# Optimization experiments

Hardware: AMD Instinct MI355X
Metric: run time of the kernel (lower is better)

Reference implementation:

```python
import jax, jax.numpy as jnp
import numpy as np

B, N, D = 4, 2048, 1024
H, DH = 16, 64
MAX_POS_EMB = 256
TOPK = 64


def setup_inputs() -> dict:
    key = jax.random.key(0)
    ks = jax.random.split(key, 8)
    s = 0.02
    inner = H * DH
    return {
        "x": jax.random.normal(ks[0], (B, N, D), jnp.float32),
        "gating_mask": jax.random.uniform(ks[1], (B, 1, N, 1), jnp.float32),
        "Wq": jax.random.normal(ks[2], (D, inner), jnp.float32) * s,
        "bq": jnp.zeros((inner,), jnp.float32),
        "Wkv": jax.random.normal(ks[3], (D, 2 * inner), jnp.float32) * s,
        "bkv": jnp.zeros((2 * inner,), jnp.float32),
        "Wo": jax.random.normal(ks[4], (inner, D), jnp.float32) * s,
        "bo": jnp.zeros((D,), jnp.float32),
        "rel_emb": jax.random.normal(ks[5], (MAX_POS_EMB, DH), jnp.float32) * s,
        "mask": jnp.ones((B, N), bool),
        "sparse_topk": TOPK,
    }


def reference(x, gating_mask, Wq, bq, Wkv, bkv, Wo, bo, rel_emb, mask, sparse_topk):
    b, n, d = x.shape
    h, dh = H, DH
    scale = dh ** -0.5
    mask_val = -jnp.finfo(x.dtype).max

    # projections -> [b, h, n, dh]
    q = (x @ Wq + bq).reshape(b, n, h, dh).transpose(0, 2, 1, 3)
    kv = x @ Wkv + bkv
    k = kv[..., : h * dh].reshape(b, n, h, dh).transpose(0, 2, 1, 3)
    v = kv[..., h * dh:].reshape(b, n, h, dh).transpose(0, 2, 1, 3)

    dots = jnp.einsum("bhid,bhjd->bhij", q, k) * scale  # [b,h,n,n]

    # relative positional bias: q . E[clip(i-j+M, 0, M-1)]
    seq = jnp.arange(n)
    dist = jnp.clip(seq[:, None] - seq[None, :] + MAX_POS_EMB, 0, MAX_POS_EMB - 1)
    qE = jnp.einsum("bhid,rd->bhir", q, rel_emb) * scale  # [b,h,n,R]
    pos_attn = jnp.take_along_axis(qE, dist[None, None, :, :], axis=-1)  # [b,h,n,n]
    dots = dots + pos_attn

    # padding mask: mask_i * mask_j
    full_mask = mask[:, None, :, None] & mask[:, None, None, :]
    dots = jnp.where(full_mask, dots, mask_val)

    # topk sparsification: keep only scores >= k-th largest per row
    top = jax.lax.top_k(dots, sparse_topk)[0]  # [b,h,n,topk]
    vk = top[..., -1:]
    dots = jnp.where(dots < vk, mask_val, dots)

    attn = jax.nn.softmax(dots, axis=-1)
    attn = attn * gating_mask

    out = jnp.einsum("bhij,bhjd->bhid", attn, v)
    out = out.transpose(0, 2, 1, 3).reshape(b, n, h * dh)
    return out @ Wo + bo
```

## Files before the change

kernel.cpp:

```cpp
#include <hip/hip_runtime.h>
#include <stdint.h>


typedef __attribute__((ext_vector_type(8))) short short8;
typedef __attribute__((ext_vector_type(4))) float floatx4;

#define Bn   4
#define Nn   2048
#define Hn   16
#define BHn  (Bn*Hn)
#define DELTA 0.00125f

__device__ __forceinline__ float bf2f(unsigned short u) {
  union { unsigned int i; float f; } v; v.i = ((unsigned int)u) << 16; return v.f;
}
__device__ __forceinline__ unsigned short f2bf(float f) {
  union { float f; unsigned int i; } v; v.f = f;
  unsigned int r = v.i + 0x7fffu + ((v.i >> 16) & 1u);
  return (unsigned short)(r >> 16);
}
__device__ __forceinline__ floatx4 mfma16(short8 a, short8 b, floatx4 c) {
  return __builtin_amdgcn_mfma_f32_16x16x32_bf16(a, b, c, 0, 0, 0);
}
__device__ __forceinline__ void split2(float x, unsigned short& h, unsigned short& m) {
  h = f2bf(x);
  m = f2bf(x - bf2f(h));
}
__device__ __forceinline__ void split3(float x, unsigned short& h, unsigned short& m, unsigned short& l) {
  h = f2bf(x);
  float r = x - bf2f(h);
  m = f2bf(r);
  l = f2bf(r - bf2f(m));
}

__global__ __launch_bounds__(256)
void transpose_split3(const float* __restrict__ W,
                      unsigned short* __restrict__ T0,
                      unsigned short* __restrict__ T1,
                      unsigned short* __restrict__ T2,
                      int K, int Ncols)
{
  __shared__ float tile[32][33];
  int k0 = blockIdx.y * 32, n0 = blockIdx.x * 32;
  int tx = threadIdx.x & 31, ty = threadIdx.x >> 5;
  for (int s = 0; s < 32; s += 8)
    tile[ty + s][tx] = W[(size_t)(k0 + ty + s) * Ncols + n0 + tx];
  __syncthreads();
  for (int s = 0; s < 32; s += 8) {
    float x = tile[tx][ty + s];
    unsigned short h, m, l;
    split3(x, h, m, l);
    size_t o = (size_t)(n0 + ty + s) * K + k0 + tx;
    T0[o] = h; T1[o] = m; T2[o] = l;
  }
}

__global__ __launch_bounds__(256)
void transpose_split2(const float* __restrict__ W,
                      unsigned short* __restrict__ T0,
                      unsigned short* __restrict__ T1,
                      int K, int Ncols)
{
  __shared__ float tile[32][33];
  int k0 = blockIdx.y * 32, n0 = blockIdx.x * 32;
  int tx = threadIdx.x & 31, ty = threadIdx.x >> 5;
  for (int s = 0; s < 32; s += 8)
    tile[ty + s][tx] = W[(size_t)(k0 + ty + s) * Ncols + n0 + tx];
  __syncthreads();
  for (int s = 0; s < 32; s += 8) {
    float x = tile[tx][ty + s];
    unsigned short h, m;
    split2(x, h, m);
    size_t o = (size_t)(n0 + ty + s) * K + k0 + tx;
    T0[o] = h; T1[o] = m;
  }
}

__global__ __launch_bounds__(256)
void convert_bf16(const float* __restrict__ in, unsigned short* __restrict__ outp, int n) {
  int i = blockIdx.x * 256 + threadIdx.x;
  if (i < n) outp[i] = f2bf(in[i]);
}

__global__ __launch_bounds__(256)
void gemm_qkv(const float* __restrict__ A,
              const unsigned short* __restrict__ B0,
              const unsigned short* __restrict__ B1,
              const unsigned short* __restrict__ B2,
              const float* __restrict__ bias,
              float* __restrict__ O32,
              unsigned short* __restrict__ Oh,
              unsigned short* __restrict__ Om,
              unsigned short* __restrict__ Vh,
              int K, float scale)
{
  __shared__ unsigned short lA[3][128 * 40];
  __shared__ unsigned short lB[3][128 * 40];
  const int tid = threadIdx.x;
  const int lane = tid & 63;
  const int m0 = blockIdx.y * 128, n0 = blockIdx.x * 128;
  const int wid = tid >> 6, wm = wid >> 1, wn = wid & 1;
  const int fr = lane & 15, fq = lane >> 4;
  floatx4 acc[4][4] = {};

  for (int k0 = 0; k0 < K; k0 += 32) {
    __syncthreads();
    #pragma unroll
    for (int p = 0; p < 2; p++) {
      int c = tid + p * 256;
      int row = c >> 2, kc = (c & 3) * 8;
      size_t go = (size_t)(m0 + row) * K + k0 + kc;
      float4 v0 = *(const float4*)&A[go];
      float4 v1 = *(const float4*)&A[go + 4];
      union { unsigned short u[8]; uint4 q; } hh, mm, ll;
      float xs[8] = {v0.x, v0.y, v0.z, v0.w, v1.x, v1.y, v1.z, v1.w};
      #pragma unroll
      for (int e = 0; e < 8; e++) split3(xs[e], hh.u[e], mm.u[e], ll.u[e]);
      *(uint4*)&lA[0][row * 40 + kc] = hh.q;
      *(uint4*)&lA[1][row * 40 + kc] = mm.q;
      *(uint4*)&lA[2][row * 40 + kc] = ll.q;
      size_t bo = (size_t)(n0 + row) * K + k0 + kc;
      *(uint4*)&lB[0][row * 40 + kc] = *(const uint4*)&B0[bo];
      *(uint4*)&lB[1][row * 40 + kc] = *(const uint4*)&B1[bo];
      *(uint4*)&lB[2][row * 40 + kc] = *(const uint4*)&B2[bo];
    }
    __syncthreads();
    short8 af[3][4], bfr[3][4];
    #pragma unroll
    for (int s = 0; s < 3; s++)
      #pragma unroll
      for (int t = 0; t < 4; t++) {
        af[s][t]  = *(const short8*)&lA[s][(wm * 64 + t * 16 + fr) * 40 + 8 * fq];
        bfr[s][t] = *(const short8*)&lB[s][(wn * 64 + t * 16 + fr) * 40 + 8 * fq];
      }
    #pragma unroll
    for (int mi = 0; mi < 4; mi++)
      #pragma unroll
      for (int ni = 0; ni < 4; ni++) {
        acc[mi][ni] = mfma16(af[0][mi], bfr[0][ni], acc[mi][ni]);
        acc[mi][ni] = mfma16(af[0][mi], bfr[1][ni], acc[mi][ni]);
        acc[mi][ni] = mfma16(af[1][mi], bfr[0][ni], acc[mi][ni]);
        acc[mi][ni] = mfma16(af[1][mi], bfr[1][ni], acc[mi][ni]);
        acc[mi][ni] = mfma16(af[0][mi], bfr[2][ni], acc[mi][ni]);
        acc[mi][ni] = mfma16(af[2][mi], bfr[0][ni], acc[mi][ni]);
      }
  }
  #pragma unroll
  for (int mi = 0; mi < 4; mi++)
    #pragma unroll
    for (int ni = 0; ni < 4; ni++) {
      int nl = n0 + wn * 64 + ni * 16 + fr;
      float bv = bias[nl];
      #pragma unroll
      for (int rg = 0; rg < 4; rg++) {
        int ml = m0 + wm * 64 + mi * 16 + fq * 4 + rg;
        float val = (acc[mi][ni][rg] + bv) * scale;
        int bb = ml >> 11, ii = ml & 2047;
        int hh2 = (nl & 1023) >> 6, dd = nl & 63;
        size_t idx = (((size_t)bb * Hn + hh2) * Nn + ii) * 64 + dd;
        if (nl < 1024) {
          O32[idx] = val;
          unsigned short h, m;
          split2(val, h, m);
          Oh[idx] = h; Om[idx] = m;
        } else {
          Vh[idx] = f2bf(val);
        }
      }
    }
}

__global__ __launch_bounds__(256)
void gemm_out(const float* __restrict__ A,
              const unsigned short* __restrict__ B0,
              const unsigned short* __restrict__ B1,
              const float* __restrict__ bias,
              float* __restrict__ O32,
              int Ncols, int K)
{
  __shared__ unsigned short lA[2][128 * 40];
  __shared__ unsigned short lB[2][128 * 40];
  const int tid = threadIdx.x;
  const int lane = tid & 63;
  const int m0 = blockIdx.y * 128, n0 = blockIdx.x * 128;
  const int wid = tid >> 6, wm = wid >> 1, wn = wid & 1;
  const int fr = lane & 15, fq = lane >> 4;
  floatx4 acc[4][4] = {};

  for (int k0 = 0; k0 < K; k0 += 32) {
    __syncthreads();
    #pragma unroll
    for (int p = 0; p < 2; p++) {
      int c = tid + p * 256;
      int row = c >> 2, kc = (c & 3) * 8;
      size_t go = (size_t)(m0 + row) * K + k0 + kc;
      float4 v0 = *(const float4*)&A[go];
      float4 v1 = *(const float4*)&A[go + 4];
      union { unsigned short u[8]; uint4 q; } hh, mm;
      float xs[8] = {v0.x, v0.y, v0.z, v0.w, v1.x, v1.y, v1.z, v1.w};
      #pragma unroll
      for (int e = 0; e < 8; e++) split2(xs[e], hh.u[e], mm.u[e]);
      *(uint4*)&lA[0][row * 40 + kc] = hh.q;
      *(uint4*)&lA[1][row * 40 + kc] = mm.q;
      size_t bo = (size_t)(n0 + row) * K + k0 + kc;
      *(uint4*)&lB[0][row * 40 + kc] = *(const uint4*)&B0[bo];
      *(uint4*)&lB[1][row * 40 + kc] = *(const uint4*)&B1[bo];
    }
    __syncthreads();
    short8 af[2][4], bfr[2][4];
    #pragma unroll
    for (int s = 0; s < 2; s++)
      #pragma unroll
      for (int t = 0; t < 4; t++) {
        af[s][t]  = *(const short8*)&lA[s][(wm * 64 + t * 16 + fr) * 40 + 8 * fq];
        bfr[s][t] = *(const short8*)&lB[s][(wn * 64 + t * 16 + fr) * 40 + 8 * fq];
      }
    #pragma unroll
    for (int mi = 0; mi < 4; mi++)
      #pragma unroll
      for (int ni = 0; ni < 4; ni++) {
        acc[mi][ni] = mfma16(af[0][mi], bfr[0][ni], acc[mi][ni]);
        acc[mi][ni] = mfma16(af[0][mi], bfr[1][ni], acc[mi][ni]);
        acc[mi][ni] = mfma16(af[1][mi], bfr[0][ni], acc[mi][ni]);
      }
  }
  #pragma unroll
  for (int mi = 0; mi < 4; mi++)
    #pragma unroll
    for (int ni = 0; ni < 4; ni++) {
      int nl = n0 + wn * 64 + ni * 16 + fr;
      float bv = bias[nl];
      #pragma unroll
      for (int rg = 0; rg < 4; rg++) {
        int ml = m0 + wm * 64 + mi * 16 + fq * 4 + rg;
        O32[(size_t)ml * Ncols + nl] = acc[mi][ni][rg] + bv;
      }
    }
}

__global__ __launch_bounds__(512, 4)
void attn_k(const unsigned short* __restrict__ qh,
            const unsigned short* __restrict__ qm,
            const unsigned short* __restrict__ kh,
            const unsigned short* __restrict__ km,
            const unsigned short* __restrict__ vh,
            const float* __restrict__ q32,
            const float* __restrict__ k32,
            const unsigned short* __restrict__ relbf,
            const float* __restrict__ rel32,
            const float* __restrict__ gating,
            const int* __restrict__ topkp,
            float* __restrict__ inner)
{
  extern __shared__ char smem[];
  _Float16* S = (_Float16*)smem;
  unsigned short* KtH = (unsigned short*)(smem + 65536);
  unsigned short* KtM = KtH + 4096;
  _Float16* qE = (_Float16*)KtH;

  const int ib = blockIdx.x, bh = blockIdx.y;
  const int i0 = ib * 16;
  const int b = bh >> 4, h = bh & 15;
  const int tid = threadIdx.x;
  const int lane = tid & 63, w = tid >> 6;
  const int fr = lane & 15, fq = lane >> 4;
  const int topk = topkp[0];

  const size_t qoff = ((size_t)bh * Nn + i0) * 64;
  const size_t qf = qoff + (size_t)fr * 64 + 8 * fq;
  const short8 aqh0 = *(const short8*)&qh[qf];
  const short8 aqh1 = *(const short8*)&qh[qf + 32];
  const short8 aqm0 = *(const short8*)&qm[qf];
  const short8 aqm1 = *(const short8*)&qm[qf + 32];

  for (int jt = 0; jt < 32; jt++) {
    __syncthreads();
    {
      int row = tid >> 3, dc = (tid & 7) * 8;
      size_t g = ((size_t)bh * Nn + jt * 64 + row) * 64 + dc;
      *(uint4*)&KtH[row * 64 + dc] = *(const uint4*)&kh[g];
      *(uint4*)&KtM[row * 64 + dc] = *(const uint4*)&km[g];
    }
    __syncthreads();
    if ((jt & 1) == (w >> 2)) {
      int wc = w & 3;
      int kb = (wc * 16 + fr) * 64 + 8 * fq;
      short8 kh0 = *(const short8*)&KtH[kb];
      short8 kh1 = *(const short8*)&KtH[kb + 32];
      short8 km0 = *(const short8*)&KtM[kb];
      short8 km1 = *(const short8*)&KtM[kb + 32];
      floatx4 c = {};
      c = mfma16(aqh0, kh0, c); c = mfma16(aqh1, kh1, c);
      c = mfma16(aqh0, km0, c); c = mfma16(aqh1, km1, c);
      c = mfma16(aqm0, kh0, c); c = mfma16(aqm1, kh1, c);
      #pragma unroll
      for (int rg = 0; rg < 4; rg++)
        S[(fq * 4 + rg) * 2048 + jt * 64 + wc * 16 + fr] = (_Float16)c[rg];
    }
  }
  __syncthreads();

  #pragma unroll
  for (int rs = 0; rs < 2; rs++) {
    int r0 = (w * 2 + rs) * 16;
    size_t rf = (size_t)(r0 + fr) * 64 + 8 * fq;
    short8 rb0 = *(const short8*)&relbf[rf];
    short8 rb1 = *(const short8*)&relbf[rf + 32];
    floatx4 c = {};
    c = mfma16(aqh0, rb0, c); c = mfma16(aqh1, rb1, c);
    c = mfma16(aqm0, rb0, c); c = mfma16(aqm1, rb1, c);
    #pragma unroll
    for (int rg = 0; rg < 4; rg++)
      qE[(fq * 4 + rg) * 256 + r0 + fr] = (_Float16)c[rg];
  }
  __syncthreads();

  #pragma unroll 1
  for (int rr = 0; rr < 2; rr++) {
    const int r = w * 2 + rr;
    const int i = i0 + r;
    const _Float16* Srow = S + r * 2048;
    const _Float16* qErow = qE + r * 256;

    float key[32];
    float mx = -3.0e38f, sum = 0.f, ssq = 0.f;
    #pragma unroll
    for (int e = 0; e < 16; e++) {
      int j0 = 2 * lane + 128 * e;
      union { unsigned int u; _Float16 hx[2]; } sv;
      sv.u = *(const unsigned int*)&Srow[j0];
      int r0i = i - j0 + 256;
      int c0 = r0i < 0 ? 0 : (r0i > 255 ? 255 : r0i);
      int r1i = r0i - 1;
      int c1 = r1i < 0 ? 0 : (r1i > 255 ? 255 : r1i);
      float s0 = (float)sv.hx[0] + (float)qErow[c0];
      float s1 = (float)sv.hx[1] + (float)qErow[c1];
      key[2 * e] = s0; key[2 * e + 1] = s1;
      mx = fmaxf(mx, fmaxf(s0, s1));
      sum += s0 + s1;
      ssq += s0 * s0 + s1 * s1;
    }
    #pragma unroll
    for (int d = 1; d < 64; d <<= 1) {
      mx = fmaxf(mx, __shfl_xor(mx, d));
      sum += __shfl_xor(sum, d);
      ssq += __shfl_xor(ssq, d);
    }
    const float mu = sum * (1.f / 2048.f);
    const float sg = sqrtf(fmaxf(ssq * (1.f / 2048.f) - mu * mu, 0.f)) + 1e-9f;

    auto cntGE = [&](float u) -> int {
      int c = 0;
      #pragma unroll
      for (int e = 0; e < 32; e++) c += (key[e] >= u) ? 1 : 0;
      #pragma unroll
      for (int d = 1; d < 64; d <<= 1) c += __shfl_xor(c, d);
      return c;
    };

    float lo = mu + 1.6f * sg;
    float hi = mx + fabsf(mx) * 1e-6f + 1e-20f;
    int cl = cntGE(lo);
    #pragma unroll 1
    for (int t = 0; t < 6 && cl < topk; t++) {
      hi = lo; lo -= (0.8f + 0.4f * t) * sg; cl = cntGE(lo);
    }
    if (cl < topk) lo = -3.0e38f;
    #pragma unroll 1
    for (int it = 0; it < 10; it++) {
      float mid = 0.5f * (lo + hi);
      if (cntGE(mid) >= topk) lo = mid; else hi = mid;
    }
    const float C = hi + 2.0f * DELTA;
    const float L = lo - 2.0f * DELTA;

    char* sb = (char*)Srow;
    float* Pl = (float*)(sb);
    int*   Jl = (int*)(sb + 512);
    float* Sx = (float*)(sb + 1024);
    int*   Jc = (int*)(sb + 1280);
    asm volatile("" ::: "memory");
    const unsigned long long lmlt = (1ull << lane) - 1ull;

    int base = 0;
    #pragma unroll
    for (int e2 = 0; e2 < 32; e2++) {
      bool dk = key[e2] >= C;
      unsigned long long mk = __ballot(dk);
      if (dk) {
        int pos = base + __popcll(mk & lmlt);
        Pl[pos] = key[e2]; Jl[pos] = 2 * lane + 128 * (e2 >> 1) + (e2 & 1);
      }
      base += __popcll(mk);
    }
    int mcand = 0;
    #pragma unroll
    for (int e2 = 0; e2 < 32; e2++) {
      bool cd = (key[e2] >= L) && (key[e2] < C);
      unsigned long long mk = __ballot(cd);
      if (cd) {
        int pos = mcand + __popcll(mk & lmlt);
        if (pos < 64) Jc[pos] = 2 * lane + 128 * (e2 >> 1) + (e2 & 1);
      }
      mcand += __popcll(mk);
    }
    if (mcand > 64) mcand = 64;
    asm volatile("" ::: "memory");

    const size_t qrow = ((size_t)bh * Nn + i) * 64 + lane;
    const double qv = (double)q32[qrow];
    #pragma unroll 1
    for (int c2 = 0; c2 < mcand; c2++) {
      int j = Jc[c2];
      int ridx = i - j + 256;
      ridx = ridx < 0 ? 0 : (ridx > 255 ? 255 : ridx);
      size_t krow = ((size_t)bh * Nn + j) * 64 + lane;
      double t = qv * ((double)k32[krow] + (double)rel32[ridx * 64 + lane]);
      #pragma unroll
      for (int d = 1; d < 64; d <<= 1) t += __shfl_xor(t, d);
      if (lane == 0) Sx[c2] = (float)t;
    }
    asm volatile("" ::: "memory");

    const int need = topk - base;
    float myx = (lane < mcand) ? Sx[lane] : -3.0e38f;
    int rank = 0;
    #pragma unroll 1
    for (int c2 = 0; c2 < mcand; c2++) {
      float o = Sx[c2];
      rank += (o > myx || (o == myx && c2 < lane)) ? 1 : 0;
    }
    bool ck = (lane < mcand) && (rank < need);
    unsigned long long mk2 = __ballot(ck);
    if (ck) {
      int pos = base + __popcll(mk2 & lmlt);
      Pl[pos] = myx; Jl[pos] = Jc[lane];
    }
    base += __popcll(mk2);
    const int nk = base;
    asm volatile("" ::: "memory");

    float p = 0.f;
    if (lane < nk) { p = __expf(Pl[lane] - mx); Pl[lane] = p; }
    float psum = p;
    #pragma unroll
    for (int d = 1; d < 64; d <<= 1) psum += __shfl_xor(psum, d);
    const float coef = gating[(size_t)b * Nn + i] / psum;
    asm volatile("" ::: "memory");

    float a0 = 0, a1 = 0, a2 = 0, a3 = 0;
    const size_t vb = (size_t)bh * Nn * 64;
    int t4 = nk & ~3;
    #pragma unroll 1
    for (int t = 0; t < t4; t += 4) {
      float p0 = Pl[t], p1 = Pl[t + 1], p2 = Pl[t + 2], p3 = Pl[t + 3];
      int j0 = Jl[t], j1 = Jl[t + 1], j2 = Jl[t + 2], j3 = Jl[t + 3];
      a0 += p0 * bf2f(vh[vb + (size_t)j0 * 64 + lane]);
      a1 += p1 * bf2f(vh[vb + (size_t)j1 * 64 + lane]);
      a2 += p2 * bf2f(vh[vb + (size_t)j2 * 64 + lane]);
      a3 += p3 * bf2f(vh[vb + (size_t)j3 * 64 + lane]);
    }
    for (int t = t4; t < nk; t++)
      a0 += Pl[t] * bf2f(vh[vb + (size_t)Jl[t] * 64 + lane]);
    float outv = (a0 + a1 + a2 + a3) * coef;
    inner[((size_t)b * Nn + i) * 1024 + h * 64 + lane] = outv;
  }
}

extern "C" void kernel_launch(void* const* d_in, const int* in_sizes, int n_in,
                              void* d_out, int out_size, void* d_ws, size_t ws_size,
                              hipStream_t stream) {
  const float* x      = (const float*)d_in[0];
  const float* gating = (const float*)d_in[1];
  const float* Wq     = (const float*)d_in[2];
  const float* bq     = (const float*)d_in[3];
  const float* Wkv    = (const float*)d_in[4];
  const float* bkv    = (const float*)d_in[5];
  const float* Wo     = (const float*)d_in[6];
  const float* bo     = (const float*)d_in[7];
  const float* rel    = (const float*)d_in[8];
  const int*   topk   = (const int*)d_in[10];
  float* out = (float*)d_out;

  char* ws = (char*)d_ws;
  size_t off = 0;
  auto alloc = [&](size_t bytes) -> void* {
    void* p = ws + off; off += (bytes + 255) & ~(size_t)255; return p;
  };
  unsigned short* Wqt0 = (unsigned short*)alloc(1024ull * 1024 * 2);
  unsigned short* Wqt1 = (unsigned short*)alloc(1024ull * 1024 * 2);
  unsigned short* Wqt2 = (unsigned short*)alloc(1024ull * 1024 * 2);
  unsigned short* Wkt0 = (unsigned short*)alloc(2048ull * 1024 * 2);
  unsigned short* Wkt1 = (unsigned short*)alloc(2048ull * 1024 * 2);
  unsigned short* Wkt2 = (unsigned short*)alloc(2048ull * 1024 * 2);
  unsigned short* Wot0 = (unsigned short*)alloc(1024ull * 1024 * 2);
  unsigned short* Wot1 = (unsigned short*)alloc(1024ull * 1024 * 2);
  unsigned short* relbf = (unsigned short*)alloc(256ull * 64 * 2);
  float* q32 = (float*)alloc((size_t)BHn * Nn * 64 * 4);
  float* k32 = (float*)alloc((size_t)BHn * Nn * 64 * 4);
  unsigned short* qhb = (unsigned short*)alloc((size_t)BHn * Nn * 64 * 2);
  unsigned short* qmb = (unsigned short*)alloc((size_t)BHn * Nn * 64 * 2);
  unsigned short* khb = (unsigned short*)alloc((size_t)BHn * Nn * 64 * 2);
  unsigned short* kmb = (unsigned short*)alloc((size_t)BHn * Nn * 64 * 2);
  unsigned short* vhb = (unsigned short*)alloc((size_t)BHn * Nn * 64 * 2);
  float* inner = (float*)alloc((size_t)Bn * Nn * 1024 * 4);
  if (off > ws_size) return;

  size_t shmem = 65536 + 16384;
  (void)hipFuncSetAttribute((const void*)attn_k,
                            hipFuncAttributeMaxDynamicSharedMemorySize, (int)shmem);

  transpose_split3<<<dim3(32, 32), 256, 0, stream>>>(Wq, Wqt0, Wqt1, Wqt2, 1024, 1024);
  transpose_split3<<<dim3(64, 32), 256, 0, stream>>>(Wkv, Wkt0, Wkt1, Wkt2, 1024, 2048);
  transpose_split2<<<dim3(32, 32), 256, 0, stream>>>(Wo, Wot0, Wot1, 1024, 1024);
  convert_bf16<<<dim3(64), 256, 0, stream>>>(rel, relbf, 256 * 64);

  gemm_qkv<<<dim3(8, 64), 256, 0, stream>>>(x, Wqt0, Wqt1, Wqt2, bq,
      q32, qhb, qmb, qhb, 1024, 0.125f);
  gemm_qkv<<<dim3(16, 64), 256, 0, stream>>>(x, Wkt0, Wkt1, Wkt2, bkv,
      k32, khb, kmb, vhb, 1024, 1.0f);

  attn_k<<<dim3(128, 64), 512, shmem, stream>>>(qhb, qmb, khb, kmb, vhb,
      q32, k32, relbf, rel, gating, topk, inner);

  gemm_out<<<dim3(8, 64), 256, 0, stream>>>(inner, Wot0, Wot1, bo,
      out, 1024, 1024);
}
```

Before: 1.294 ms.

## Widen attention blocks to 1024 threads, swizzle LDS, trim V-GEMM precision passes

The attention kernel now launches 1024 threads, with one row per wave instead of two per wave. It adds XOR swizzling on the K tiles, the score matrix and the qE buffer in shared memory to cut bank conflicts. It also uses a shortcut for clamped relative-position entries, simplifies the threshold search bracketing, and includes ties at the k-th value. Separately, the V half of the QKV GEMM drops the third-split MFMA passes and stores V as fp16 instead of bf16, which reduces the GEMM's compute and loads. The changes trade some precision in V, plus register pressure from the larger blocks, for more parallelism and fewer LDS conflicts.

```diff
diff --git a/kernel.cpp b/kernel.cpp
--- a/kernel.cpp
+++ b/kernel.cpp
@@ -91,7 +91,7 @@
               float* __restrict__ O32,
               unsigned short* __restrict__ Oh,
               unsigned short* __restrict__ Om,
-              unsigned short* __restrict__ Vh,
+              _Float16* __restrict__ Vh,
               int K, float scale)
 {
   __shared__ unsigned short lA[3][128 * 40];
@@ -99,6 +99,7 @@
   const int tid = threadIdx.x;
   const int lane = tid & 63;
   const int m0 = blockIdx.y * 128, n0 = blockIdx.x * 128;
+  const bool vblk = (n0 >= 1024);
   const int wid = tid >> 6, wm = wid >> 1, wn = wid & 1;
   const int fr = lane & 15, fq = lane >> 4;
   floatx4 acc[4][4] = {};
@@ -118,31 +119,41 @@
       for (int e = 0; e < 8; e++) split3(xs[e], hh.u[e], mm.u[e], ll.u[e]);
       *(uint4*)&lA[0][row * 40 + kc] = hh.q;
       *(uint4*)&lA[1][row * 40 + kc] = mm.q;
-      *(uint4*)&lA[2][row * 40 + kc] = ll.q;
       size_t bo = (size_t)(n0 + row) * K + k0 + kc;
       *(uint4*)&lB[0][row * 40 + kc] = *(const uint4*)&B0[bo];
       *(uint4*)&lB[1][row * 40 + kc] = *(const uint4*)&B1[bo];
-      *(uint4*)&lB[2][row * 40 + kc] = *(const uint4*)&B2[bo];
+      if (!vblk) {
+        *(uint4*)&lA[2][row * 40 + kc] = ll.q;
+        *(uint4*)&lB[2][row * 40 + kc] = *(const uint4*)&B2[bo];
+      }
     }
     __syncthreads();
-    short8 af[3][4], bfr[3][4];
-    #pragma unroll
-    for (int s = 0; s < 3; s++)
-      #pragma unroll
-      for (int t = 0; t < 4; t++) {
-        af[s][t]  = *(const short8*)&lA[s][(wm * 64 + t * 16 + fr) * 40 + 8 * fq];
-        bfr[s][t] = *(const short8*)&lB[s][(wn * 64 + t * 16 + fr) * 40 + 8 * fq];
-      }
+    short8 af0[4], af1[4], af2[4], bf0[4], bf1[4], bf2v[4];
+    #pragma unroll
+    for (int t = 0; t < 4; t++) {
+      int ao = (wm * 64 + t * 16 + fr) * 40 + 8 * fq;
+      int bo2 = (wn * 64 + t * 16 + fr) * 40 + 8 * fq;
+      af0[t] = *(const short8*)&lA[0][ao];
+      af1[t] = *(const short8*)&lA[1][ao];
+      bf0[t] = *(const short8*)&lB[0][bo2];
+      bf1[t] = *(const short8*)&lB[1][bo2];
+      if (!vblk) {
+        af2[t] = *(const short8*)&lA[2][ao];
+        bf2v[t] = *(const short8*)&lB[2][bo2];
+      }
+    }
     #pragma unroll
     for (int mi = 0; mi < 4; mi++)
       #pragma unroll
       for (int ni = 0; ni < 4; ni++) {
-        acc[mi][ni] = mfma16(af[0][mi], bfr[0][ni], acc[mi][ni]);
-        acc[mi][ni] = mfma16(af[0][mi], bfr[1][ni], acc[mi][ni]);
-        acc[mi][ni] = mfma16(af[1][mi], bfr[0][ni], acc[mi][ni]);
-        acc[mi][ni] = mfma16(af[1][mi], bfr[1][ni], acc[mi][ni]);
-        acc[mi][ni] = mfma16(af[0][mi], bfr[2][ni], acc[mi][ni]);
-        acc[mi][ni] = mfma16(af[2][mi], bfr[0][ni], acc[mi][ni]);
+        acc[mi][ni] = mfma16(af0[mi], bf0[ni], acc[mi][ni]);
+        acc[mi][ni] = mfma16(af0[mi], bf1[ni], acc[mi][ni]);
+        acc[mi][ni] = mfma16(af1[mi], bf0[ni], acc[mi][ni]);
+        if (!vblk) {
+          acc[mi][ni] = mfma16(af1[mi], bf1[ni], acc[mi][ni]);
+          acc[mi][ni] = mfma16(af0[mi], bf2v[ni], acc[mi][ni]);
+          acc[mi][ni] = mfma16(af2[mi], bf0[ni], acc[mi][ni]);
+        }
       }
   }
   #pragma unroll
@@ -158,13 +169,13 @@
         int bb = ml >> 11, ii = ml & 2047;
         int hh2 = (nl & 1023) >> 6, dd = nl & 63;
         size_t idx = (((size_t)bb * Hn + hh2) * Nn + ii) * 64 + dd;
-        if (nl < 1024) {
+        if (!vblk) {
           O32[idx] = val;
           unsigned short h, m;
           split2(val, h, m);
           Oh[idx] = h; Om[idx] = m;
         } else {
-          Vh[idx] = f2bf(val);
+          Vh[idx] = (_Float16)val;
         }
       }
     }
@@ -238,12 +249,12 @@
     }
 }
 
-__global__ __launch_bounds__(512, 4)
+__global__ __launch_bounds__(1024, 8)
 void attn_k(const unsigned short* __restrict__ qh,
             const unsigned short* __restrict__ qm,
             const unsigned short* __restrict__ kh,
             const unsigned short* __restrict__ km,
-            const unsigned short* __restrict__ vh,
+            const _Float16* __restrict__ vh,
             const float* __restrict__ q32,
             const float* __restrict__ k32,
             const unsigned short* __restrict__ relbf,
@@ -276,195 +287,185 @@
   for (int jt = 0; jt < 32; jt++) {
     __syncthreads();
     {
-      int row = tid >> 3, dc = (tid & 7) * 8;
-      size_t g = ((size_t)bh * Nn + jt * 64 + row) * 64 + dc;
-      *(uint4*)&KtH[row * 64 + dc] = *(const uint4*)&kh[g];
-      *(uint4*)&KtM[row * 64 + dc] = *(const uint4*)&km[g];
+      int sel = tid >> 9;
+      int row = (tid >> 3) & 63, ch = tid & 7;
+      int dst = row * 64 + ((ch ^ (row & 7)) * 8);
+      size_t g = ((size_t)bh * Nn + jt * 64 + row) * 64 + ch * 8;
+      unsigned short* T = sel ? KtM : KtH;
+      const unsigned short* src = sel ? km : kh;
+      *(uint4*)&T[dst] = *(const uint4*)&src[g];
     }
     __syncthreads();
-    if ((jt & 1) == (w >> 2)) {
+    if (w < 8 && ((jt & 1) == (w >> 2))) {
       int wc = w & 3;
-      int kb = (wc * 16 + fr) * 64 + 8 * fq;
-      short8 kh0 = *(const short8*)&KtH[kb];
-      short8 kh1 = *(const short8*)&KtH[kb + 32];
-      short8 km0 = *(const short8*)&KtM[kb];
-      short8 km1 = *(const short8*)&KtM[kb + 32];
+      int row16 = wc * 16 + fr, r7 = fr & 7;
+      int b0 = row16 * 64 + ((fq ^ r7) * 8);
+      int b1 = row16 * 64 + (((fq + 4) ^ r7) * 8);
+      short8 kh0 = *(const short8*)&KtH[b0];
+      short8 kh1 = *(const short8*)&KtH[b1];
+      short8 km0 = *(const short8*)&KtM[b0];
+      short8 km1 = *(const short8*)&KtM[b1];
       floatx4 c = {};
       c = mfma16(aqh0, kh0, c); c = mfma16(aqh1, kh1, c);
       c = mfma16(aqh0, km0, c); c = mfma16(aqh1, km1, c);
       c = mfma16(aqm0, kh0, c); c = mfma16(aqm1, kh1, c);
+      int colsw = jt * 64 + ((wc ^ fq) * 16) + fr;
       #pragma unroll
       for (int rg = 0; rg < 4; rg++)
-        S[(fq * 4 + rg) * 2048 + jt * 64 + wc * 16 + fr] = (_Float16)c[rg];
+        S[(fq * 4 + rg) * 2048 + colsw] = (_Float16)c[rg];
     }
   }
   __syncthreads();
 
-  #pragma unroll
-  for (int rs = 0; rs < 2; rs++) {
-    int r0 = (w * 2 + rs) * 16;
-    size_t rf = (size_t)(r0 + fr) * 64 + 8 * fq;
+  {
+    size_t rf = (size_t)(w * 16 + fr) * 64 + 8 * fq;
     short8 rb0 = *(const short8*)&relbf[rf];
     short8 rb1 = *(const short8*)&relbf[rf + 32];
     floatx4 c = {};
     c = mfma16(aqh0, rb0, c); c = mfma16(aqh1, rb1, c);
     c = mfma16(aqm0, rb0, c); c = mfma16(aqm1, rb1, c);
+    int colsw = ((w ^ fq) * 16) + fr;
     #pragma unroll
     for (int rg = 0; rg < 4; rg++)
-      qE[(fq * 4 + rg) * 256 + r0 + fr] = (_Float16)c[rg];
+      qE[(fq * 4 + rg) * 256 + colsw] = (_Float16)c[rg];
   }
   __syncthreads();
 
+  const int r = w;
+  const int i = i0 + r;
+  const int X = (r >> 2) << 4;
+  _Float16* S0 = S + r * 2048;
+  const _Float16* qE0 = qE + r * 256;
+  const float cA = (float)qE0[255 ^ X], cC = (float)qE0[X];
+  const int swl = (2 * lane) ^ X;
+
+  float key[32];
+  float mx = -3.0e38f, sm = 0.f, sq = 0.f;
+  #pragma unroll
+  for (int e = 0; e < 16; e++) {
+    const int jb = 128 * e;
+    union { unsigned int u; _Float16 hx[2]; } u0;
+    u0.u = *(const unsigned int*)&S0[jb + swl];
+    const int j0 = jb + 2 * lane;
+    float e0, e1;
+    if (jb + 127 <= i) { e0 = cA; e1 = cA; }
+    else if (jb >= i + 256) { e0 = cC; e1 = cC; }
+    else {
+      int c0 = i - j0 + 256; c0 = c0 < 0 ? 0 : (c0 > 255 ? 255 : c0);
+      int c1 = i - j0 + 255; c1 = c1 < 0 ? 0 : (c1 > 255 ? 255 : c1);
+      e0 = (float)qE0[c0 ^ X]; e1 = (float)qE0[c1 ^ X];
+    }
+    float a0 = (float)u0.hx[0] + e0, a1 = (float)u0.hx[1] + e1;
+    key[2 * e] = a0; key[2 * e + 1] = a1;
+    mx = fmaxf(mx, fmaxf(a0, a1));
+    sm += a0 + a1;
+    sq = fmaf(a0, a0, fmaf(a1, a1, sq));
+  }
+  #pragma unroll
+  for (int d = 1; d < 64; d <<= 1) {
+    mx = fmaxf(mx, __shfl_xor(mx, d));
+    sm += __shfl_xor(sm, d);
+    sq += __shfl_xor(sq, d);
+  }
+  const float mu = sm * (1.f / 2048.f);
+  const float sg = sqrtf(fmaxf(sq * (1.f / 2048.f) - mu * mu, 0.f)) + 1e-9f;
+
+  auto cntGE = [&](float u) -> int {
+    int c = 0;
+    #pragma unroll
+    for (int t = 0; t < 32; t++) c += (key[t] >= u) ? 1 : 0;
+    #pragma unroll
+    for (int d = 1; d < 64; d <<= 1) c += __shfl_xor(c, d);
+    return c;
+  };
+
+  float lo = mu + 1.6f * sg;
+  float hi = mx + fabsf(mx) * 1e-6f + 1e-20f;
+  if (cntGE(lo) < topk) {
+    lo = mu;
+    if (cntGE(lo) < topk) lo = mu - 20.f * sg;
+  }
   #pragma unroll 1
-  for (int rr = 0; rr < 2; rr++) {
-    const int r = w * 2 + rr;
-    const int i = i0 + r;
-    const _Float16* Srow = S + r * 2048;
-    const _Float16* qErow = qE + r * 256;
-
-    float key[32];
-    float mx = -3.0e38f, sum = 0.f, ssq = 0.f;
-    #pragma unroll
-    for (int e = 0; e < 16; e++) {
-      int j0 = 2 * lane + 128 * e;
-      union { unsigned int u; _Float16 hx[2]; } sv;
-      sv.u = *(const unsigned int*)&Srow[j0];
-      int r0i = i - j0 + 256;
-      int c0 = r0i < 0 ? 0 : (r0i > 255 ? 255 : r0i);
-      int r1i = r0i - 1;
-      int c1 = r1i < 0 ? 0 : (r1i > 255 ? 255 : r1i);
-      float s0 = (float)sv.hx[0] + (float)qErow[c0];
-      float s1 = (float)sv.hx[1] + (float)qErow[c1];
-      key[2 * e] = s0; key[2 * e + 1] = s1;
-      mx = fmaxf(mx, fmaxf(s0, s1));
-      sum += s0 + s1;
-      ssq += s0 * s0 + s1 * s1;
-    }
-    #pragma unroll
-    for (int d = 1; d < 64; d <<= 1) {
-      mx = fmaxf(mx, __shfl_xor(mx, d));
-      sum += __shfl_xor(sum, d);
-      ssq += __shfl_xor(ssq, d);
-    }
-    const float mu = sum * (1.f / 2048.f);
-    const float sg = sqrtf(fmaxf(ssq * (1.f / 2048.f) - mu * mu, 0.f)) + 1e-9f;
-
-    auto cntGE = [&](float u) -> int {
-      int c = 0;
-      #pragma unroll
-      for (int e = 0; e < 32; e++) c += (key[e] >= u) ? 1 : 0;
-      #pragma unroll
-      for (int d = 1; d < 64; d <<= 1) c += __shfl_xor(c, d);
-      return c;
-    };
-
-    float lo = mu + 1.6f * sg;
-    float hi = mx + fabsf(mx) * 1e-6f + 1e-20f;
-    int cl = cntGE(lo);
-    #pragma unroll 1
-    for (int t = 0; t < 6 && cl < topk; t++) {
-      hi = lo; lo -= (0.8f + 0.4f * t) * sg; cl = cntGE(lo);
-    }
-    if (cl < topk) lo = -3.0e38f;
-    #pragma unroll 1
-    for (int it = 0; it < 10; it++) {
-      float mid = 0.5f * (lo + hi);
-      if (cntGE(mid) >= topk) lo = mid; else hi = mid;
-    }
-    const float C = hi + 2.0f * DELTA;
-    const float L = lo - 2.0f * DELTA;
-
-    char* sb = (char*)Srow;
-    float* Pl = (float*)(sb);
-    int*   Jl = (int*)(sb + 512);
-    float* Sx = (float*)(sb + 1024);
-    int*   Jc = (int*)(sb + 1280);
-    asm volatile("" ::: "memory");
-    const unsigned long long lmlt = (1ull << lane) - 1ull;
-
-    int base = 0;
-    #pragma unroll
-    for (int e2 = 0; e2 < 32; e2++) {
-      bool dk = key[e2] >= C;
-      unsigned long long mk = __ballot(dk);
-      if (dk) {
-        int pos = base + __popcll(mk & lmlt);
-        Pl[pos] = key[e2]; Jl[pos] = 2 * lane + 128 * (e2 >> 1) + (e2 & 1);
-      }
-      base += __popcll(mk);
-    }
-    int mcand = 0;
-    #pragma unroll
-    for (int e2 = 0; e2 < 32; e2++) {
-      bool cd = (key[e2] >= L) && (key[e2] < C);
-      unsigned long long mk = __ballot(cd);
-      if (cd) {
-        int pos = mcand + __popcll(mk & lmlt);
-        if (pos < 64) Jc[pos] = 2 * lane + 128 * (e2 >> 1) + (e2 & 1);
-      }
-      mcand += __popcll(mk);
-    }
-    if (mcand > 64) mcand = 64;
-    asm volatile("" ::: "memory");
-
-    const size_t qrow = ((size_t)bh * Nn + i) * 64 + lane;
-    const double qv = (double)q32[qrow];
-    #pragma unroll 1
-    for (int c2 = 0; c2 < mcand; c2++) {
-      int j = Jc[c2];
-      int ridx = i - j + 256;
-      ridx = ridx < 0 ? 0 : (ridx > 255 ? 255 : ridx);
-      size_t krow = ((size_t)bh * Nn + j) * 64 + lane;
-      double t = qv * ((double)k32[krow] + (double)rel32[ridx * 64 + lane]);
-      #pragma unroll
-      for (int d = 1; d < 64; d <<= 1) t += __shfl_xor(t, d);
-      if (lane == 0) Sx[c2] = (float)t;
-    }
-    asm volatile("" ::: "memory");
-
-    const int need = topk - base;
-    float myx = (lane < mcand) ? Sx[lane] : -3.0e38f;
-    int rank = 0;
-    #pragma unroll 1
-    for (int c2 = 0; c2 < mcand; c2++) {
-      float o = Sx[c2];
-      rank += (o > myx || (o == myx && c2 < lane)) ? 1 : 0;
-    }
-    bool ck = (lane < mcand) && (rank < need);
-    unsigned long long mk2 = __ballot(ck);
-    if (ck) {
-      int pos = base + __popcll(mk2 & lmlt);
-      Pl[pos] = myx; Jl[pos] = Jc[lane];
-    }
-    base += __popcll(mk2);
-    const int nk = base;
-    asm volatile("" ::: "memory");
-
-    float p = 0.f;
-    if (lane < nk) { p = __expf(Pl[lane] - mx); Pl[lane] = p; }
-    float psum = p;
-    #pragma unroll
-    for (int d = 1; d < 64; d <<= 1) psum += __shfl_xor(psum, d);
-    const float coef = gating[(size_t)b * Nn + i] / psum;
-    asm volatile("" ::: "memory");
-
-    float a0 = 0, a1 = 0, a2 = 0, a3 = 0;
-    const size_t vb = (size_t)bh * Nn * 64;
-    int t4 = nk & ~3;
-    #pragma unroll 1
-    for (int t = 0; t < t4; t += 4) {
-      float p0 = Pl[t], p1 = Pl[t + 1], p2 = Pl[t + 2], p3 = Pl[t + 3];
-      int j0 = Jl[t], j1 = Jl[t + 1], j2 = Jl[t + 2], j3 = Jl[t + 3];
-      a0 += p0 * bf2f(vh[vb + (size_t)j0 * 64 + lane]);
-      a1 += p1 * bf2f(vh[vb + (size_t)j1 * 64 + lane]);
-      a2 += p2 * bf2f(vh[vb + (size_t)j2 * 64 + lane]);
-      a3 += p3 * bf2f(vh[vb + (size_t)j3 * 64 + lane]);
-    }
-    for (int t = t4; t < nk; t++)
-      a0 += Pl[t] * bf2f(vh[vb + (size_t)Jl[t] * 64 + lane]);
-    float outv = (a0 + a1 + a2 + a3) * coef;
-    inner[((size_t)b * Nn + i) * 1024 + h * 64 + lane] = outv;
-  }
+  for (int it = 0; it < 10; it++) {
+    float mid = 0.5f * (lo + hi);
+    if (cntGE(mid) >= topk) lo = mid; else hi = mid;
+  }
+  const float C = hi + 2.f * DELTA, L = lo - 2.f * DELTA;
+
+  char* sb = (char*)S0;
+  float* Pl = (float*)sb;          int* Jl = (int*)(sb + 512);
+  float* Sx = (float*)(sb + 1024); int* Jc = (int*)(sb + 1280);
+  asm volatile("" ::: "memory");
+  const unsigned long long lmlt = (1ull << lane) - 1ull;
+
+  int base = 0, mc = 0;
+  #pragma unroll
+  for (int t = 0; t < 32; t++) {
+    const int j = 2 * lane + 128 * (t >> 1) + (t & 1);
+    bool dk = key[t] >= C;
+    bool cd = (key[t] >= L) && !dk;
+    unsigned long long mk = __ballot(dk);
+    if (dk) { int pos = base + __popcll(mk & lmlt); Pl[pos] = key[t]; Jl[pos] = j; }
+    base += __popcll(mk);
+    mk = __ballot(cd);
+    if (cd) { int pos = mc + __popcll(mk & lmlt); if (pos < 64) Jc[pos] = j; }
+    mc += __popcll(mk);
+  }
+  if (mc > 64) mc = 64;
+  asm volatile("" ::: "memory");
+
+  const double qv = (double)q32[((size_t)bh * Nn + i) * 64 + lane];
+  #pragma unroll 1
+  for (int c2 = 0; c2 < mc; c2++) {
+    int j = Jc[c2];
+    int ridx = i - j + 256; ridx = ridx < 0 ? 0 : (ridx > 255 ? 255 : ridx);
+    double t = qv * ((double)k32[((size_t)bh * Nn + j) * 64 + lane] +
+                     (double)rel32[ridx * 64 + lane]);
+    #pragma unroll
+    for (int d = 1; d < 64; d <<= 1) t += __shfl_xor(t, d);
+    if (lane == 0) Sx[c2] = (float)t;
+  }
+  asm volatile("" ::: "memory");
+
+  const int need = topk - base;
+  float myx = (lane < mc) ? Sx[lane] : -3.0e38f;
+  int rank = 0;
+  #pragma unroll 1
+  for (int c2 = 0; c2 < mc; c2++) {
+    float o = Sx[c2];
+    rank += (o > myx || (o == myx && c2 < lane)) ? 1 : 0;
+  }
+  unsigned long long bm = __ballot((lane < mc) && (rank == need - 1));
+  float vk = bm ? __shfl(myx, (int)__ffsll(bm) - 1) : 3.0e38f;
+  bool ck = (lane < mc) && ((rank < need) || (myx == vk));
+  unsigned long long km2 = __ballot(ck);
+  if (ck) { int pos = base + __popcll(km2 & lmlt); Pl[pos] = myx; Jl[pos] = Jc[lane]; }
+  const int nk = base + __popcll(km2);
+  asm volatile("" ::: "memory");
+
+  float ps = 0.f;
+  #pragma unroll 1
+  for (int t = lane; t < nk; t += 64) { float p = __expf(Pl[t] - mx); Pl[t] = p; ps += p; }
+  #pragma unroll
+  for (int d = 1; d < 64; d <<= 1) ps += __shfl_xor(ps, d);
+  const float coef = gating[(size_t)b * Nn + i] / ps;
+  asm volatile("" ::: "memory");
+
+  const _Float16* vbp = vh + (size_t)bh * Nn * 64 + lane;
+  float a0 = 0.f, a1 = 0.f, a2 = 0.f, a3 = 0.f;
+  int t4 = nk & ~3;
+  #pragma unroll 1
+  for (int t = 0; t < t4; t += 4) {
+    float p0 = Pl[t], p1 = Pl[t + 1], p2 = Pl[t + 2], p3 = Pl[t + 3];
+    int j0 = Jl[t], j1 = Jl[t + 1], j2 = Jl[t + 2], j3 = Jl[t + 3];
+    a0 += p0 * (float)vbp[(size_t)j0 * 64];
+    a1 += p1 * (float)vbp[(size_t)j1 * 64];
+    a2 += p2 * (float)vbp[(size_t)j2 * 64];
+    a3 += p3 * (float)vbp[(size_t)j3 * 64];
+  }
+  #pragma unroll 1
+  for (int t = t4; t < nk; t++) a0 += Pl[t] * (float)vbp[(size_t)Jl[t] * 64];
+  inner[((size_t)b * Nn + i) * 1024 + h * 64 + lane] = (a0 + a1 + a2 + a3) * coef;
 }
 
 extern "C" void kernel_launch(void* const* d_in, const int* in_sizes, int n_in,
@@ -502,7 +503,7 @@
   unsigned short* qmb = (unsigned short*)alloc((size_t)BHn * Nn * 64 * 2);
   unsigned short* khb = (unsigned short*)alloc((size_t)BHn * Nn * 64 * 2);
   unsigned short* kmb = (unsigned short*)alloc((size_t)BHn * Nn * 64 * 2);
-  unsigned short* vhb = (unsigned short*)alloc((size_t)BHn * Nn * 64 * 2);
+  _Float16* vhb = (_Float16*)alloc((size_t)BHn * Nn * 64 * 2);
   float* inner = (float*)alloc((size_t)Bn * Nn * 1024 * 4);
   if (off > ws_size) return;
 
@@ -516,11 +517,11 @@
   convert_bf16<<<dim3(64), 256, 0, stream>>>(rel, relbf, 256 * 64);
 
   gemm_qkv<<<dim3(8, 64), 256, 0, stream>>>(x, Wqt0, Wqt1, Wqt2, bq,
-      q32, qhb, qmb, qhb, 1024, 0.125f);
+      q32, qhb, qmb, vhb, 1024, 0.125f);
   gemm_qkv<<<dim3(16, 64), 256, 0, stream>>>(x, Wkt0, Wkt1, Wkt2, bkv,
       k32, khb, kmb, vhb, 1024, 1.0f);
 
-  attn_k<<<dim3(128, 64), 512, shmem, stream>>>(qhb, qmb, khb, kmb, vhb,
+  attn_k<<<dim3(128, 64), 1024, shmem, stream>>>(qhb, qmb, khb, kmb, vhb,
       q32, k32, relbf, rel, gating, topk, inner);
 
   gemm_out<<<dim3(8, 64), 256, 0, stream>>>(inner, Wot0, Wot1, bo,
```

Measured after the change: 1.174 ms. 9.3% less time.
